# Kernel tuning notes

Hardware: AMD Instinct MI355X
Metric: run time of the kernel (lower is better)

## Reference

```python
import jax, jax.numpy as jnp
import numpy as np

EMBED_DIM = 1024
NUM_HEADS = 16
D_K = EMBED_DIM // NUM_HEADS
BATCH, SEQ = 4, 2048


def setup_inputs() -> dict:
    key = jax.random.key(0)
    ks = jax.random.split(key, 6)
    s = 1.0 / np.sqrt(EMBED_DIM)
    return {
        "x": jax.random.normal(ks[0], (BATCH, SEQ, EMBED_DIM), dtype=jnp.float32),
        "mask": jnp.ones((BATCH, SEQ), dtype=jnp.int32),
        "Wq": jax.random.uniform(ks[1], (EMBED_DIM, EMBED_DIM), jnp.float32, -s, s),
        "Wk": jax.random.uniform(ks[2], (EMBED_DIM, EMBED_DIM), jnp.float32, -s, s),
        "Wv": jax.random.uniform(ks[3], (EMBED_DIM, EMBED_DIM), jnp.float32, -s, s),
        "Wo": jax.random.uniform(ks[4], (EMBED_DIM, EMBED_DIM), jnp.float32, -s, s),
    }


def reference(x, mask, Wq, Wk, Wv, Wo):
    B, S, E = x.shape
    H, Dk = NUM_HEADS, D_K
    # nn.Linear: y = x @ W.T ; reshape to [B, H, S, Dk]
    def proj(W):
        return jnp.einsum('bse,fe->bsf', x, W).reshape(B, S, H, Dk).transpose(0, 2, 1, 3)
    q, k, v = proj(Wq), proj(Wk), proj(Wv)
    scores = jnp.einsum('bhqd,bhkd->bhqk', q, k) / jnp.sqrt(jnp.float32(Dk))
    # key-padding mask: [B, S] -> [B, 1, 1, S]; 0 means masked with -inf
    scores = jnp.where(mask[:, None, None, :] == 0, -jnp.inf, scores)
    attn = jax.nn.softmax(scores, axis=-1)  # dropout is identity (p=0 / eval)
    out = jnp.einsum('bhqk,bhkd->bhqd', attn, v)
    out = out.transpose(0, 2, 1, 3).reshape(B, S, E)
    return jnp.einsum('bse,fe->bsf', out, Wo)
```

## Files before the change

### kernel.cpp

```cpp
#include <hip/hip_runtime.h>

typedef __attribute__((ext_vector_type(8))) __bf16   bf16x8;
typedef __attribute__((ext_vector_type(8))) _Float16 f16x8;
typedef __attribute__((ext_vector_type(4))) _Float16 f16x4;
typedef __attribute__((ext_vector_type(4))) float    f32x4;

#define MFMA_BF16 __builtin_amdgcn_mfma_f32_16x16x32_bf16
#define MFMA_F16  __builtin_amdgcn_mfma_f32_16x16x32_f16

__global__ __launch_bounds__(256)
void cast_bf16(const float* __restrict__ src, __bf16* __restrict__ dst, int n8)
{
    int i = blockIdx.x * 256 + threadIdx.x;
    if (i >= n8) return;
    float4 v0 = *(const float4*)(src + (size_t)i * 8);
    float4 v1 = *(const float4*)(src + (size_t)i * 8 + 4);
    float xs[8] = {v0.x, v0.y, v0.z, v0.w, v1.x, v1.y, v1.z, v1.w};
    bf16x8 h8;
    #pragma unroll
    for (int j = 0; j < 8; j++) h8[j] = (__bf16)xs[j];
    *(bf16x8*)(dst + (size_t)i * 8) = h8;
}

#define GEMM_DECLS                                                          \
    __shared__ __bf16 Ah[128][40], Bh[128][40];                             \
    const int t    = threadIdx.x;                                           \
    const int lane = t & 63;                                                \
    const int wid  = t >> 6;                                                \
    const int l15  = lane & 15;                                             \
    const int lg   = lane >> 4;                                             \
    const int wr   = wid >> 1, wc = wid & 1;

#define GEMM_LOOP(Ag, Bg, m0, brow0, K)                                     \
    f32x4 acc[4][4];                                                        \
    _Pragma("unroll")                                                       \
    for (int i = 0; i < 4; i++)                                             \
        _Pragma("unroll")                                                   \
        for (int jj = 0; jj < 4; jj++)                                      \
            _Pragma("unroll")                                               \
            for (int r = 0; r < 4; r++) acc[i][jj][r] = 0.f;                \
    for (int k0 = 0; k0 < K; k0 += 32) {                                    \
        __syncthreads();                                                    \
        _Pragma("unroll")                                                   \
        for (int i = 0; i < 2; i++) {                                       \
            int id = t + 256 * i;                                           \
            int row = id >> 2, cc = id & 3;                                 \
            *(bf16x8*)&Ah[row][cc*8] =                                      \
                *(const bf16x8*)(Ag + (size_t)(m0 + row) * K + k0 + cc*8);  \
            *(bf16x8*)&Bh[row][cc*8] =                                      \
                *(const bf16x8*)(Bg + (size_t)(brow0 + row) * K + k0 + cc*8);\
        }                                                                   \
        __syncthreads();                                                    \
        bf16x8 ah[4];                                                       \
        _Pragma("unroll")                                                   \
        for (int mr = 0; mr < 4; mr++)                                      \
            ah[mr] = *(const bf16x8*)&Ah[wr*64 + mr*16 + l15][lg*8];        \
        _Pragma("unroll")                                                   \
        for (int nr = 0; nr < 4; nr++) {                                    \
            bf16x8 bh = *(const bf16x8*)&Bh[wc*64 + nr*16 + l15][lg*8];     \
            _Pragma("unroll")                                               \
            for (int mr = 0; mr < 4; mr++)                                  \
                acc[mr][nr] = MFMA_BF16(ah[mr], bh, acc[mr][nr], 0, 0, 0);  \
        }                                                                   \
    }

__global__ __launch_bounds__(256, 4)
void gemm_qkv(const __bf16* __restrict__ xh, const __bf16* __restrict__ w3,
              __bf16* __restrict__ qh, __bf16* __restrict__ kh,
              _Float16* __restrict__ vh)
{
    GEMM_DECLS
    const int K = 1024, N = 1024;
    const int m0     = blockIdx.x * 128;
    const int by     = blockIdx.y;
    const int region = by >> 3;
    const int n0     = (by & 7) * 128;
    const int brow0  = region * 1024 + n0;
    GEMM_LOOP(xh, w3, m0, brow0, K)

    #pragma unroll
    for (int mr = 0; mr < 4; mr++)
    #pragma unroll
    for (int r = 0; r < 4; r++) {
        int row = m0 + wr*64 + mr*16 + lg*4 + r;
        #pragma unroll
        for (int nr = 0; nr < 4; nr++) {
            int col = n0 + wc*64 + nr*16 + l15;
            size_t off = (size_t)row * N + col;
            float v = acc[mr][nr][r];
            if (region == 0)      qh[off] = (__bf16)(v * 0.125f);
            else if (region == 1) kh[off] = (__bf16)v;
            else                  vh[off] = (_Float16)v;
        }
    }
}

__global__ __launch_bounds__(256, 4)
void gemm_out(const __bf16* __restrict__ aoh, const __bf16* __restrict__ woh,
              float* __restrict__ out, int M, int N, int K)
{
    GEMM_DECLS
    const int m0 = blockIdx.x * 128, n0 = blockIdx.y * 128;
    GEMM_LOOP(aoh, woh, m0, n0, K)

    #pragma unroll
    for (int mr = 0; mr < 4; mr++)
    #pragma unroll
    for (int r = 0; r < 4; r++) {
        int row = m0 + wr*64 + mr*16 + lg*4 + r;
        #pragma unroll
        for (int nr = 0; nr < 4; nr++) {
            int col = n0 + wc*64 + nr*16 + l15;
            out[(size_t)row * N + col] = acc[mr][nr][r];
        }
    }
}

__global__ __launch_bounds__(256, 2)
void attn_bf16(const __bf16* __restrict__ Qg, const __bf16* __restrict__ Kg,
               const _Float16* __restrict__ Vg, const int* __restrict__ mask,
               __bf16* AO)
{
    const int S = 2048, E = 1024;
    __shared__ __bf16   Kh[64][72];
    __shared__ _Float16 Vt[64][72];
    __shared__ _Float16 Ps[128][72];

    const int tid  = threadIdx.x;
    const int lane = tid & 63;
    const int wid  = tid >> 6;
    const int l15  = lane & 15;
    const int lg   = lane >> 4;

    const int fid = blockIdx.x;
    const int xcd = fid & 7;
    const int j   = fid >> 3;
    const int bh  = xcd * 8 + (j >> 4);
    const int qb  = j & 15;
    const int h   = bh & 15;
    const int b   = bh >> 4;
    const int q0  = qb * 128;
    const size_t base = (size_t)b * S * E + (size_t)h * 64;

    bf16x8 qf[2][2];
    #pragma unroll
    for (int mg = 0; mg < 2; mg++) {
        size_t qoff = base + (size_t)(q0 + wid*32 + mg*16 + l15) * E;
        #pragma unroll
        for (int kc = 0; kc < 2; kc++)
            qf[mg][kc] = *(const bf16x8*)(Qg + qoff + kc*32 + lg*8);
    }

    f32x4 o[2][4];
    float lpart[2][4];
    #pragma unroll
    for (int mg = 0; mg < 2; mg++)
        #pragma unroll
        for (int nt = 0; nt < 4; nt++) {
            #pragma unroll
            for (int r = 0; r < 4; r++) o[mg][nt][r] = 0.f;
            lpart[mg][nt] = 0.f;
        }

    bf16x8 kpre[2]; f16x8 vpre[2];
    #pragma unroll
    for (int i = 0; i < 2; i++) {
        int id = tid + 256 * i, row = id >> 3, scc = id & 7;
        size_t g0 = base + (size_t)(row) * E + scc * 8;
        kpre[i] = *(const bf16x8*)(Kg + g0);
        vpre[i] = *(const f16x8*)(Vg + g0);
    }

    const int NT = S / 64;
    for (int t = 0; t < NT; t++) {
        const int k0 = t * 64;
        __syncthreads();

        #pragma unroll
        for (int i = 0; i < 2; i++) {
            int id = tid + 256 * i, row = id >> 3, scc = id & 7;
            *(bf16x8*)&Kh[(row & 3) * 16 + (row >> 2)][scc*8] = kpre[i];
            int cbase = ((row >> 3) ^ scc) * 8 + (row & 7);
            #pragma unroll
            for (int jj = 0; jj < 8; jj++)
                Vt[scc*8 + jj][cbase] = vpre[i][jj];
        }

        if (t + 1 < NT) {
            #pragma unroll
            for (int i = 0; i < 2; i++) {
                int id = tid + 256 * i, row = id >> 3, scc = id & 7;
                size_t gn = base + (size_t)(k0 + 64 + row) * E + scc * 8;
                kpre[i] = *(const bf16x8*)(Kg + gn);
                vpre[i] = *(const f16x8*)(Vg + gn);
            }
        }
        __syncthreads();

        f32x4 sf[2][4];
        #pragma unroll
        for (int mg = 0; mg < 2; mg++)
            #pragma unroll
            for (int nt = 0; nt < 4; nt++)
                #pragma unroll
                for (int r = 0; r < 4; r++) sf[mg][nt][r] = 0.f;

        #pragma unroll
        for (int kc = 0; kc < 2; kc++)
            #pragma unroll
            for (int nt = 0; nt < 4; nt++) {
                bf16x8 kb = *(const bf16x8*)&Kh[nt*16 + l15][kc*32 + lg*8];
                #pragma unroll
                for (int mg = 0; mg < 2; mg++)
                    sf[mg][nt] = MFMA_BF16(qf[mg][kc], kb, sf[mg][nt], 0, 0, 0);
            }

        int4 mk4 = *(const int4*)(mask + b * S + k0 + l15 * 4);
        int mk[4] = {mk4.x, mk4.y, mk4.z, mk4.w};

        #pragma unroll
        for (int mg = 0; mg < 2; mg++)
            #pragma unroll
            for (int r = 0; r < 4; r++) {
                int rowp = wid*32 + mg*16 + lg*4 + r;
                f16x4 pv4;
                #pragma unroll
                for (int nt = 0; nt < 4; nt++) {
                    float p = mk[nt] ? __expf(sf[mg][nt][r]) : 0.f;
                    lpart[mg][r] += p;
                    pv4[nt] = (_Float16)p;
                }
                *(f16x4*)&Ps[rowp][l15 * 4] = pv4;
            }

        asm volatile("s_waitcnt lgkmcnt(0)" ::: "memory");
        __builtin_amdgcn_sched_barrier(0);

        #pragma unroll
        for (int kc = 0; kc < 2; kc++) {
            f16x8 pa0 = *(const f16x8*)&Ps[wid*32 +      l15][kc*32 + lg*8];
            f16x8 pa1 = *(const f16x8*)&Ps[wid*32 + 16 + l15][kc*32 + lg*8];
            #pragma unroll
            for (int nt = 0; nt < 4; nt++) {
                int c8p = (kc*4 + lg) ^ (nt*2 + (l15 >> 3));
                f16x8 vb = *(const f16x8*)&Vt[nt*16 + l15][c8p*8];
                o[0][nt] = MFMA_F16(pa0, vb, o[0][nt], 0, 0, 0);
                o[1][nt] = MFMA_F16(pa1, vb, o[1][nt], 0, 0, 0);
            }
        }
    }

    float inv[2][4];
    #pragma unroll
    for (int mg = 0; mg < 2; mg++)
        #pragma unroll
        for (int r = 0; r < 4; r++) {
            float l = lpart[mg][r];
            #pragma unroll
            for (int d = 1; d < 16; d <<= 1) l += __shfl_xor(l, d, 16);
            inv[mg][r] = 1.0f / l;
        }

    unsigned short* Pu = (unsigned short*)&Ps[0][0];
    __syncthreads();
    #pragma unroll
    for (int mg = 0; mg < 2; mg++)
        #pragma unroll
        for (int r = 0; r < 4; r++)
            #pragma unroll
            for (int nt = 0; nt < 4; nt++) {
                __bf16 v = (__bf16)(o[mg][nt][r] * inv[mg][r]);
                Pu[(wid*32 + mg*16 + lg*4 + r) * 72 + nt*16 + l15] =
                    *(unsigned short*)&v;
            }
    __syncthreads();
    #pragma unroll
    for (int i = 0; i < 4; i++) {
        int u   = tid + 256 * i;
        int row = u >> 3, c8 = u & 7;
        bf16x8 v8;
        #pragma unroll
        for (int jj = 0; jj < 8; jj++) {
            unsigned short us = Pu[row * 72 + c8*8 + jj];
            v8[jj] = *(__bf16*)&us;
        }
        *(bf16x8*)(AO + base + (size_t)(q0 + row) * E + c8 * 8) = v8;
    }
}

extern "C" void kernel_launch(void* const* d_in, const int* in_sizes, int n_in,
                              void* d_out, int out_size, void* d_ws, size_t ws_size,
                              hipStream_t stream)
{
    const float* x    = (const float*)d_in[0];
    const int*   mask = (const int*)  d_in[1];
    const float* Wq   = (const float*)d_in[2];
    const float* Wk   = (const float*)d_in[3];
    const float* Wv   = (const float*)d_in[4];
    const float* Wo   = (const float*)d_in[5];
    float* out = (float*)d_out;

    const int B = 4, S = 2048, E = 1024;
    const int M = B * S;
    const size_t SZ  = (size_t)M * E;
    const size_t WSZ = (size_t)E * E;
    const size_t PB  = SZ * sizeof(__bf16);

    char* ws = (char*)d_ws;
    __bf16*   qh = (__bf16*)(ws);
    __bf16*   kh = (__bf16*)(ws + PB);
    _Float16* vh = (_Float16*)(ws + 2*PB);
    __bf16*   xh = (__bf16*)(ws + 3*PB);
    __bf16*   w3 = (__bf16*)(ws + 4*PB);
    __bf16*   wo = (__bf16*)(ws + 4*PB + 3*WSZ*sizeof(__bf16));

    const int n8x = (int)(SZ / 8);
    const int n8w = (int)(WSZ / 8);

    cast_bf16<<<n8x/256, 256, 0, stream>>>(x,  xh, n8x);
    cast_bf16<<<n8w/256, 256, 0, stream>>>(Wq, w3,           n8w);
    cast_bf16<<<n8w/256, 256, 0, stream>>>(Wk, w3 + WSZ,     n8w);
    cast_bf16<<<n8w/256, 256, 0, stream>>>(Wv, w3 + 2*WSZ,   n8w);
    cast_bf16<<<n8w/256, 256, 0, stream>>>(Wo, wo, n8w);

    gemm_qkv<<<dim3(M/128, 24), dim3(256), 0, stream>>>(xh, w3, qh, kh, vh);

    attn_bf16<<<dim3(1024), dim3(256), 0, stream>>>(qh, kh, vh, mask, qh);

    gemm_out<<<dim3(M/128, E/128), dim3(256), 0, stream>>>(qh, wo, out, M, E, E);
}
```

Measured before the change: 218.5 us.

## Fold log2e into Q scale, precompute mask bias, compute row sums via MFMA

Q is now scaled by 0.125*log2(e) so the softmax can use the raw exp2 instruction, and the key mask is turned into an additive bias precomputed by a small kernel and fed in as the MFMA accumulator's initial value. The row sum of probabilities is no longer accumulated with scalar adds and shuffles; a row of ones is appended to the V tile in LDS and an extra MFMA produces the sums. P is packed to fp16 with the round-toward-zero pack instruction. This cuts VALU work in the softmax inner loop at the cost of extra MFMAs, LDS space, and one more launch. The sum is now taken over fp16-rounded probabilities, and like the old code there is no max subtraction.

```diff
diff --git a/kernel.cpp b/kernel.cpp
--- a/kernel.cpp
+++ b/kernel.cpp
@@ -3,6 +3,8 @@
 typedef __attribute__((ext_vector_type(8))) __bf16   bf16x8;
 typedef __attribute__((ext_vector_type(8))) _Float16 f16x8;
 typedef __attribute__((ext_vector_type(4))) _Float16 f16x4;
+typedef __attribute__((ext_vector_type(2))) __fp16   h16x2;
+typedef __attribute__((ext_vector_type(4))) __fp16   h16x4;
 typedef __attribute__((ext_vector_type(4))) float    f32x4;
 
 #define MFMA_BF16 __builtin_amdgcn_mfma_f32_16x16x32_bf16
@@ -20,6 +22,13 @@
     #pragma unroll
     for (int j = 0; j < 8; j++) h8[j] = (__bf16)xs[j];
     *(bf16x8*)(dst + (size_t)i * 8) = h8;
+}
+
+__global__ __launch_bounds__(256)
+void mask_bias(const int* __restrict__ mask, float* __restrict__ bias, int n)
+{
+    int i = blockIdx.x * 256 + threadIdx.x;
+    if (i < n) bias[i] = mask[i] ? 0.f : -30000.f;
 }
 
 #define GEMM_DECLS                                                          \
@@ -78,6 +87,7 @@
     const int brow0  = region * 1024 + n0;
     GEMM_LOOP(xh, w3, m0, brow0, K)
 
+    constexpr float QSCALE = 0.18033688011112f;
     #pragma unroll
     for (int mr = 0; mr < 4; mr++)
     #pragma unroll
@@ -88,7 +98,7 @@
             int col = n0 + wc*64 + nr*16 + l15;
             size_t off = (size_t)row * N + col;
             float v = acc[mr][nr][r];
-            if (region == 0)      qh[off] = (__bf16)(v * 0.125f);
+            if (region == 0)      qh[off] = (__bf16)(v * QSCALE);
             else if (region == 1) kh[off] = (__bf16)v;
             else                  vh[off] = (_Float16)v;
         }
@@ -118,12 +128,12 @@
 
 __global__ __launch_bounds__(256, 2)
 void attn_bf16(const __bf16* __restrict__ Qg, const __bf16* __restrict__ Kg,
-               const _Float16* __restrict__ Vg, const int* __restrict__ mask,
+               const _Float16* __restrict__ Vg, const float* __restrict__ biasg,
                __bf16* AO)
 {
     const int S = 2048, E = 1024;
     __shared__ __bf16   Kh[64][72];
-    __shared__ _Float16 Vt[64][72];
+    __shared__ _Float16 Vt[80][72];
     __shared__ _Float16 Ps[128][72];
 
     const int tid  = threadIdx.x;
@@ -142,6 +152,11 @@
     const int q0  = qb * 128;
     const size_t base = (size_t)b * S * E + (size_t)h * 64;
 
+    {
+        _Float16* vones = &Vt[64][0];
+        for (int i = tid; i < 16 * 72; i += 256) vones[i] = (_Float16)1.0f;
+    }
+
     bf16x8 qf[2][2];
     #pragma unroll
     for (int mg = 0; mg < 2; mg++) {
@@ -151,16 +166,16 @@
             qf[mg][kc] = *(const bf16x8*)(Qg + qoff + kc*32 + lg*8);
     }
 
-    f32x4 o[2][4];
-    float lpart[2][4];
-    #pragma unroll
-    for (int mg = 0; mg < 2; mg++)
-        #pragma unroll
-        for (int nt = 0; nt < 4; nt++) {
+    f32x4 o[2][4], osum[2];
+    #pragma unroll
+    for (int mg = 0; mg < 2; mg++) {
+        #pragma unroll
+        for (int nt = 0; nt < 4; nt++)
             #pragma unroll
             for (int r = 0; r < 4; r++) o[mg][nt][r] = 0.f;
-            lpart[mg][nt] = 0.f;
-        }
+        #pragma unroll
+        for (int r = 0; r < 4; r++) osum[mg][r] = 0.f;
+    }
 
     bf16x8 kpre[2]; f16x8 vpre[2];
     #pragma unroll
@@ -197,13 +212,14 @@
         }
         __syncthreads();
 
+        f32x4 bias4 = *(const f32x4*)(biasg + b * S + k0 + l15 * 4);
         f32x4 sf[2][4];
         #pragma unroll
         for (int mg = 0; mg < 2; mg++)
             #pragma unroll
             for (int nt = 0; nt < 4; nt++)
                 #pragma unroll
-                for (int r = 0; r < 4; r++) sf[mg][nt][r] = 0.f;
+                for (int r = 0; r < 4; r++) sf[mg][nt][r] = bias4[nt];
 
         #pragma unroll
         for (int kc = 0; kc < 2; kc++)
@@ -215,22 +231,19 @@
                     sf[mg][nt] = MFMA_BF16(qf[mg][kc], kb, sf[mg][nt], 0, 0, 0);
             }
 
-        int4 mk4 = *(const int4*)(mask + b * S + k0 + l15 * 4);
-        int mk[4] = {mk4.x, mk4.y, mk4.z, mk4.w};
-
         #pragma unroll
         for (int mg = 0; mg < 2; mg++)
             #pragma unroll
             for (int r = 0; r < 4; r++) {
                 int rowp = wid*32 + mg*16 + lg*4 + r;
-                f16x4 pv4;
-                #pragma unroll
-                for (int nt = 0; nt < 4; nt++) {
-                    float p = mk[nt] ? __expf(sf[mg][nt][r]) : 0.f;
-                    lpart[mg][r] += p;
-                    pv4[nt] = (_Float16)p;
-                }
-                *(f16x4*)&Ps[rowp][l15 * 4] = pv4;
+                float p0 = __builtin_amdgcn_exp2f(sf[mg][0][r]);
+                float p1 = __builtin_amdgcn_exp2f(sf[mg][1][r]);
+                float p2 = __builtin_amdgcn_exp2f(sf[mg][2][r]);
+                float p3 = __builtin_amdgcn_exp2f(sf[mg][3][r]);
+                h16x2 a = __builtin_amdgcn_cvt_pkrtz(p0, p1);
+                h16x2 c = __builtin_amdgcn_cvt_pkrtz(p2, p3);
+                h16x4 pv4 = __builtin_shufflevector(a, c, 0, 1, 2, 3);
+                *(h16x4*)&Ps[rowp][l15 * 4] = pv4;
             }
 
         asm volatile("s_waitcnt lgkmcnt(0)" ::: "memory");
@@ -247,6 +260,9 @@
                 o[0][nt] = MFMA_F16(pa0, vb, o[0][nt], 0, 0, 0);
                 o[1][nt] = MFMA_F16(pa1, vb, o[1][nt], 0, 0, 0);
             }
+            f16x8 vb1 = *(const f16x8*)&Vt[64 + l15][(kc*4 + lg)*8];
+            osum[0] = MFMA_F16(pa0, vb1, osum[0], 0, 0, 0);
+            osum[1] = MFMA_F16(pa1, vb1, osum[1], 0, 0, 0);
         }
     }
 
@@ -254,12 +270,7 @@
     #pragma unroll
     for (int mg = 0; mg < 2; mg++)
         #pragma unroll
-        for (int r = 0; r < 4; r++) {
-            float l = lpart[mg][r];
-            #pragma unroll
-            for (int d = 1; d < 16; d <<= 1) l += __shfl_xor(l, d, 16);
-            inv[mg][r] = 1.0f / l;
-        }
+        for (int r = 0; r < 4; r++) inv[mg][r] = 1.0f / osum[mg][r];
 
     unsigned short* Pu = (unsigned short*)&Ps[0][0];
     __syncthreads();
@@ -313,6 +324,7 @@
     __bf16*   xh = (__bf16*)(ws + 3*PB);
     __bf16*   w3 = (__bf16*)(ws + 4*PB);
     __bf16*   wo = (__bf16*)(ws + 4*PB + 3*WSZ*sizeof(__bf16));
+    float*    bs = (float*)(ws + 4*PB + 4*WSZ*sizeof(__bf16));
 
     const int n8x = (int)(SZ / 8);
     const int n8w = (int)(WSZ / 8);
@@ -322,10 +334,11 @@
     cast_bf16<<<n8w/256, 256, 0, stream>>>(Wk, w3 + WSZ,     n8w);
     cast_bf16<<<n8w/256, 256, 0, stream>>>(Wv, w3 + 2*WSZ,   n8w);
     cast_bf16<<<n8w/256, 256, 0, stream>>>(Wo, wo, n8w);
+    mask_bias<<<(B*S)/256, 256, 0, stream>>>(mask, bs, B*S);
 
     gemm_qkv<<<dim3(M/128, 24), dim3(256), 0, stream>>>(xh, w3, qh, kh, vh);
 
-    attn_bf16<<<dim3(1024), dim3(256), 0, stream>>>(qh, kh, vh, mask, qh);
+    attn_bf16<<<dim3(1024), dim3(256), 0, stream>>>(qh, kh, vh, bs, qh);
 
     gemm_out<<<dim3(M/128, E/128), dim3(256), 0, stream>>>(qh, wo, out, M, E, E);
 }
```

New measurement: 223.7 us. 2.4% more time.
